# Optimization experiments

Hardware: AMD Instinct MI355X
Metric: run time of the kernel (lower is better)

## Reference

```python
import jax, jax.numpy as jnp
import numpy as np

N, E, G, H, D = 50000, 800000, 64, 2, 128  # nodes, edges, graphs, heads, out_channels
NEG_SLOPE_ATT = 0.2   # GATv2 default negative_slope
NEG_SLOPE_OUT = 0.01  # torch.nn.LeakyReLU default
BN_EPS = 1e-5


def setup_inputs() -> dict:
    key = jax.random.key(0)
    ks = jax.random.split(key, 12)
    x = jax.random.normal(ks[0], (N, 1), jnp.float32)
    edge_index = jax.random.randint(ks[1], (2, E), 0, N, dtype=jnp.int64)
    edge_attr = jax.random.normal(ks[2], (E,), jnp.float32)
    batch = jnp.sort(jax.random.randint(ks[3], (N,), 0, G, dtype=jnp.int64))
    # GATv2Conv params: lin_l/lin_r: Linear(1, H*D) with bias; lin_edge: Linear(1, H*D) no bias
    Wl = jax.random.normal(ks[4], (1, H * D), jnp.float32) * 0.5
    bl = jax.random.normal(ks[5], (H * D,), jnp.float32) * 0.1
    Wr = jax.random.normal(ks[6], (1, H * D), jnp.float32) * 0.5
    br = jax.random.normal(ks[7], (H * D,), jnp.float32) * 0.1
    We = jax.random.normal(ks[8], (1, H * D), jnp.float32) * 0.5
    att = jax.random.normal(ks[9], (H, D), jnp.float32) * 0.5
    bias = jax.random.normal(ks[10], (D,), jnp.float32) * 0.1
    gamma = jnp.ones((D,), jnp.float32)
    beta = jnp.zeros((D,), jnp.float32)
    return {"x": x, "edge_index": edge_index, "edge_attr": edge_attr, "batch": batch,
            "Wl": Wl, "bl": bl, "Wr": Wr, "br": br, "We": We, "att": att,
            "bias": bias, "gamma": gamma, "beta": beta}


def reference(x, edge_index, edge_attr, batch, Wl, bl, Wr, br, We, att, bias, gamma, beta):
    n = x.shape[0]
    src, dst = edge_index[0], edge_index[1]  # message flows src -> dst
    # node transforms: [N, H, D]
    xl = (x @ Wl + bl).reshape(n, H, D)  # lin_l (source side, also the message value)
    xr = (x @ Wr + br).reshape(n, H, D)  # lin_r (destination side)
    # edge feature embedding: [E, H, D]
    ee = (edge_attr[:, None] @ We).reshape(-1, H, D)
    # GATv2 scoring: leaky_relu(x_j + x_i + e), then dot with attention vector
    m = jax.nn.leaky_relu(xl[src] + xr[dst] + ee, NEG_SLOPE_ATT)  # [E, H, D]
    alpha = jnp.einsum('ehd,hd->eh', m, att)  # [E, H]
    # scatter-softmax over incoming edges per destination node
    amax = jax.ops.segment_max(alpha, dst, num_segments=n)  # [N, H]
    ea = jnp.exp(alpha - amax[dst])
    denom = jax.ops.segment_sum(ea, dst, num_segments=n)
    alpha = ea / (denom[dst] + 1e-16)
    # weighted scatter-add aggregation of x_j
    out = jax.ops.segment_sum(xl[src] * alpha[..., None], dst, num_segments=n)  # [N, H, D]
    out = out.mean(axis=1) + bias  # concat=False -> head average, then conv bias
    # BatchNorm1d in training mode (biased variance over nodes)
    mean = out.mean(axis=0)
    var = ((out - mean) ** 2).mean(axis=0)
    out = (out - mean) * jax.lax.rsqrt(var + BN_EPS) * gamma + beta
    out = jax.nn.leaky_relu(out, NEG_SLOPE_OUT)
    # graph-level scatter_add pooling
    return jax.ops.segment_sum(out, batch, num_segments=G)  # [G, D]
```

## Files before the change

### kernel.cpp

```cpp
#include <hip/hip_runtime.h>
#include <math.h>

#define NN 50000
#define NE 800000
#define NG 64

#define CB    1024
#define NBLK  782
#define NBUCK 196

static_assert(NBLK * CB >= NE, "chunk cover");
static_assert((NBUCK - 1) == (NN - 1) / 256, "bucket count");

#define WS_C     0
#define WS_ACC   16
#define WS_BNSUM (WS_ACC + 4*NN)
#define WS_BNSQ  (WS_BNSUM + 128)
#define WS_MOM   WS_BNSUM
#define WS_EX    (WS_BNSQ + 128)
#define WS_TOT   (WS_EX + 272)
#define WS_CNT   (WS_TOT + 256)
#define WS_REC0  (WS_CNT + 256*NBLK)
#define WS_SORT  (WS_REC0 + 4*NE)
#define WS_END   (WS_SORT + 4*NE)
#define WS_NEED_BYTES ((size_t)WS_END * 4 + 256)

static_assert(((WS_REC0 * 4) % 16) == 0, "rec0 16B alignment");
static_assert(((WS_SORT * 4) % 16) == 0, "sort 16B alignment");
static_assert(NE % 4 == 0, "edge unroll");

#define STEP(wl_, wr_, we_, bb_, at_, xs_, xd_, ae_, acc_)                 \
  { float tt = fmaf(we_, ae_, bb_); tt = fmaf(wr_, xd_, tt);               \
    tt = fmaf(wl_, xs_, tt); acc_ = fmaf(fabsf(tt), at_, acc_); }

#define SMEM_WEIGHTS_DECL                                                  \
  __shared__ __align__(16) float sWl[256], sWr[256], sWe[256], sB[256], sAt[256];

#define SMEM_WEIGHTS_LOAD                                                  \
  { int t_ = threadIdx.x;                                                  \
    sWl[t_] = Wl[t_]; sWr[t_] = Wr[t_]; sWe[t_] = We[t_];                  \
    sB[t_] = bl[t_] + br[t_]; sAt[t_] = att[t_]; }                         \
  __syncthreads();

#define SCORES(xs_, xd_, ae_, accA, accB, out0, out1)                      \
  { float lin0 = fmaf(c0.x, xs_, fmaf(c0.y, xd_, fmaf(c0.z, ae_, c0.w))); \
    out0 = fmaf(0.4f, accA, 0.6f * lin0);                                  \
    float lin1 = fmaf(c1.x, xs_, fmaf(c1.y, xd_, fmaf(c1.z, ae_, c1.w))); \
    out1 = fmaf(0.4f, accB, 0.6f * lin1); }

#define STEP4(c, q0, q1, q2, q3)                                           \
  STEP(wl.c, wr.c, we.c, bb.c, at.c, xs0, xd0, ae0, q0)                    \
  STEP(wl.c, wr.c, we.c, bb.c, at.c, xs1, xd1, ae1, q1)                    \
  STEP(wl.c, wr.c, we.c, bb.c, at.c, xs2, xd2, ae2, q2)                    \
  STEP(wl.c, wr.c, we.c, bb.c, at.c, xs3, xd3, ae3, q3)

#define SCORE_CORE                                                         \
  int4 s4 = *(const int4*)&ei[base];                                       \
  int4 dd4 = *(const int4*)&ei[NE + base];                                 \
  float4 ae4 = *(const float4*)&eattr[base];                               \
  float xs0 = x[s4.x], xs1 = x[s4.y], xs2 = x[s4.z], xs3 = x[s4.w];        \
  float xd0 = x[dd4.x], xd1 = x[dd4.y], xd2 = x[dd4.z], xd3 = x[dd4.w];    \
  float ae0 = ae4.x, ae1 = ae4.y, ae2 = ae4.z, ae3 = ae4.w;

#define SCORE_LOOPS                                                        \
  float a00 = 0.f, a01 = 0.f, a02 = 0.f, a03 = 0.f;                        \
  float a10 = 0.f, a11 = 0.f, a12 = 0.f, a13 = 0.f;                        \
  _Pragma("unroll 2")                                                      \
  for (int j = 0; j < 128; j += 4) {                                       \
    float4 wl = *(const float4*)&sWl[j];                                   \
    float4 wr = *(const float4*)&sWr[j];                                   \
    float4 we = *(const float4*)&sWe[j];                                   \
    float4 bb = *(const float4*)&sB[j];                                    \
    float4 at = *(const float4*)&sAt[j];                                   \
    STEP4(x, a00, a01, a02, a03)                                           \
    STEP4(y, a00, a01, a02, a03)                                           \
    STEP4(z, a00, a01, a02, a03)                                           \
    STEP4(w, a00, a01, a02, a03)                                           \
  }                                                                        \
  _Pragma("unroll 2")                                                      \
  for (int j = 128; j < 256; j += 4) {                                     \
    float4 wl = *(const float4*)&sWl[j];                                   \
    float4 wr = *(const float4*)&sWr[j];                                   \
    float4 we = *(const float4*)&sWe[j];                                   \
    float4 bb = *(const float4*)&sB[j];                                    \
    float4 at = *(const float4*)&sAt[j];                                   \
    STEP4(x, a10, a11, a12, a13)                                           \
    STEP4(y, a10, a11, a12, a13)                                           \
    STEP4(z, a10, a11, a12, a13)                                           \
    STEP4(w, a10, a11, a12, a13)                                           \
  }                                                                        \
  float4 c0 = *(const float4*)&ws[WS_C];                                   \
  float4 c1 = *(const float4*)&ws[WS_C + 4];

extern "C" __global__ __launch_bounds__(256)
void k0_init(float* __restrict__ ws,
             const float* __restrict__ att, const float* __restrict__ Wl,
             const float* __restrict__ Wr, const float* __restrict__ We,
             const float* __restrict__ bl, const float* __restrict__ br,
             float* __restrict__ out, int dense)
{
  int tid = blockIdx.x * 256 + threadIdx.x;
  int nt = gridDim.x * 256;
  if (dense) {
    if (tid < 14) ws[WS_MOM + tid] = 0.f;
  } else {
    for (int i = tid; i < 4 * NN; i += nt) ws[WS_ACC + i] = 0.f;
    for (int i = tid; i < 256; i += nt) ws[WS_BNSUM + i] = 0.f;
  }
  for (int i = tid; i < NG * 128; i += nt) out[i] = 0.f;
  if (blockIdx.x == 0) {
    __shared__ float red[4][256];
    int t = threadIdx.x;
    float a = att[t];
    red[0][t] = a * Wl[t];
    red[1][t] = a * Wr[t];
    red[2][t] = a * We[t];
    red[3][t] = a * (bl[t] + br[t]);
    __syncthreads();
    if (t < 8) {
      int k = t >> 1, h = t & 1;
      float s = 0.f;
      for (int d = 0; d < 128; ++d) s += red[k][h * 128 + d];
      ws[WS_C + h * 4 + k] = s;
    }
  }
}

extern "C" __global__ __launch_bounds__(256, 2)
void k_score(const int* __restrict__ ei, const float* __restrict__ x,
             const float* __restrict__ eattr,
             const float* __restrict__ Wl, const float* __restrict__ Wr,
             const float* __restrict__ We, const float* __restrict__ bl,
             const float* __restrict__ br, const float* __restrict__ att,
             float* __restrict__ ws)
{
  SMEM_WEIGHTS_DECL
  __shared__ unsigned cnt[256];
  cnt[threadIdx.x] = 0u;
  SMEM_WEIGHTS_LOAD
  int base = (blockIdx.x * 256 + threadIdx.x) * 4;
  if (base < NE) {
    SCORE_CORE
    atomicAdd(&cnt[((unsigned)dd4.x) >> 8], 1u);
    atomicAdd(&cnt[((unsigned)dd4.y) >> 8], 1u);
    atomicAdd(&cnt[((unsigned)dd4.z) >> 8], 1u);
    atomicAdd(&cnt[((unsigned)dd4.w) >> 8], 1u);
    SCORE_LOOPS
    float4* rec0 = (float4*)(ws + WS_REC0);
    float s0, s1;
    SCORES(xs0, xd0, ae0, a00, a10, s0, s1)
    rec0[base + 0] = make_float4(__expf(s0), __expf(s1), xs0, __uint_as_float((unsigned)dd4.x));
    SCORES(xs1, xd1, ae1, a01, a11, s0, s1)
    rec0[base + 1] = make_float4(__expf(s0), __expf(s1), xs1, __uint_as_float((unsigned)dd4.y));
    SCORES(xs2, xd2, ae2, a02, a12, s0, s1)
    rec0[base + 2] = make_float4(__expf(s0), __expf(s1), xs2, __uint_as_float((unsigned)dd4.z));
    SCORES(xs3, xd3, ae3, a03, a13, s0, s1)
    rec0[base + 3] = make_float4(__expf(s0), __expf(s1), xs3, __uint_as_float((unsigned)dd4.w));
  }
  __syncthreads();
  unsigned* counts = (unsigned*)(ws + WS_CNT);
  counts[(size_t)threadIdx.x * NBLK + blockIdx.x] = cnt[threadIdx.x];
}

extern "C" __global__ __launch_bounds__(256)
void k_scan1(float* __restrict__ ws)
{
  int b = blockIdx.x;
  int t = threadIdx.x;
  unsigned* row = (unsigned*)(ws + WS_CNT) + (size_t)b * NBLK;
  __shared__ unsigned sc[256];
  unsigned carry = 0;
  for (int c = 0; c < NBLK; c += 256) {
    int k = c + t;
    unsigned v = (k < NBLK) ? row[k] : 0u;
    sc[t] = v;
    __syncthreads();
    for (int o = 1; o < 256; o <<= 1) {
      unsigned u = (t >= o) ? sc[t - o] : 0u;
      __syncthreads();
      sc[t] += u;
      __syncthreads();
    }
    unsigned incl = sc[t];
    if (k < NBLK) row[k] = carry + incl - v;
    unsigned total = sc[255];
    __syncthreads();
    carry += total;
  }
  if (t == 0) ((unsigned*)(ws + WS_TOT))[b] = carry;
}

extern "C" __global__ __launch_bounds__(256)
void k_scan2(float* __restrict__ ws)
{
  int b = threadIdx.x;
  unsigned v = ((const unsigned*)(ws + WS_TOT))[b];
  __shared__ unsigned sc[256];
  sc[b] = v;
  __syncthreads();
  for (int o = 1; o < 256; o <<= 1) {
    unsigned u = (b >= o) ? sc[b - o] : 0u;
    __syncthreads();
    sc[b] += u;
    __syncthreads();
  }
  unsigned* ex = (unsigned*)(ws + WS_EX);
  ex[b] = sc[b] - v;
  if (b == 255) ex[256] = sc[b];
}

extern "C" __global__ __launch_bounds__(256)
void k_scatter(float* __restrict__ ws)
{
  __shared__ unsigned soff[256];
  int blk = blockIdx.x, tid = threadIdx.x;
  const unsigned* counts = (const unsigned*)(ws + WS_CNT);
  const unsigned* ex = (const unsigned*)(ws + WS_EX);
  soff[tid] = ex[tid] + counts[(size_t)tid * NBLK + blk];
  __syncthreads();
  const float4* rec0 = (const float4*)(ws + WS_REC0);
  float4* srt = (float4*)(ws + WS_SORT);
  int e0i = blk * CB + tid;
#pragma unroll
  for (int i = 0; i < 4; ++i) {
    int e = e0i + i * 256;
    if (e < NE) {
      float4 r = rec0[e];
      unsigned d = __float_as_uint(r.w);
      unsigned p = atomicAdd(&soff[d >> 8], 1u);
      srt[p] = r;
    }
  }
}

extern "C" __global__ __launch_bounds__(256)
void k_gather(float* __restrict__ ws)
{
  int b = blockIdx.x;
  const int t = threadIdx.x;
  __shared__ float acc[1024];
  acc[t] = 0.f; acc[256 + t] = 0.f; acc[512 + t] = 0.f; acc[768 + t] = 0.f;
  __syncthreads();
  const unsigned* ex = (const unsigned*)(ws + WS_EX);
  int lo = (int)ex[b], hi = (int)ex[b + 1];
  const float4* srt = (const float4*)(ws + WS_SORT);
  for (int i = lo + t; i < hi; i += 256) {
    float4 r = srt[i];
    int l4 = (int)(__float_as_uint(r.w) & 255u) * 4;
    atomicAdd(&acc[l4 + 0], r.x);
    atomicAdd(&acc[l4 + 1], r.y);
    atomicAdd(&acc[l4 + 2], r.x * r.z);
    atomicAdd(&acc[l4 + 3], r.y * r.z);
  }
  __syncthreads();
  int n = (b << 8) + t;
  float f1 = 0.f, f2 = 0.f, f3 = 0.f, f4 = 0.f;
  if (n < NN) {
    float4 A = make_float4(acc[t * 4], acc[t * 4 + 1], acc[t * 4 + 2], acc[t * 4 + 3]);
    *(float4*)&ws[WS_ACC + 4 * n] = A;
    float r0 = 1.f / (A.x + 1e-16f);
    float r1 = 1.f / (A.y + 1e-16f);
    f1 = A.x * r0; f2 = A.z * r0; f3 = A.y * r1; f4 = A.w * r1;
  }
  float pm[14] = { f1, f2, f3, f4,
                   f1*f1, f1*f2, f1*f3, f1*f4,
                   f2*f2, f2*f3, f2*f4,
                   f3*f3, f3*f4, f4*f4 };
#pragma unroll
  for (int k = 0; k < 14; ++k) {
    float v = pm[k];
#pragma unroll
    for (int m = 32; m >= 1; m >>= 1) v += __shfl_xor(v, m);
    pm[k] = v;
  }
  __shared__ float smom[56];
  int wid = t >> 6, lane = t & 63;
  if (lane == 0) {
#pragma unroll
    for (int k = 0; k < 14; ++k) smom[wid * 14 + k] = pm[k];
  }
  __syncthreads();
  if (t < 14) {
    float s = smom[t] + smom[14 + t] + smom[28 + t] + smom[42 + t];
    atomicAdd(&ws[WS_MOM + t], s);
  }
}

extern "C" __global__ __launch_bounds__(256)
void k4m_pool(const int* __restrict__ batch,
              const float* __restrict__ Wl, const float* __restrict__ bl,
              const float* __restrict__ bias, const float* __restrict__ gamma,
              const float* __restrict__ beta,
              float* __restrict__ ws, float* __restrict__ out)
{
  const int CHUNK = (NN + (int)gridDim.x - 1) / (int)gridDim.x;
  int n0 = blockIdx.x * CHUNK;
  if (n0 >= NN) return;
  int n1 = n0 + CHUNK; if (n1 > NN) n1 = NN;
  int t = threadIdx.x;
  int d = t & 127;
  int row = t >> 7;
  float S1 = ws[WS_MOM + 0], S2 = ws[WS_MOM + 1];
  float S3 = ws[WS_MOM + 2], S4 = ws[WS_MOM + 3];
  float M11 = ws[WS_MOM + 4], M12 = ws[WS_MOM + 5], M13 = ws[WS_MOM + 6];
  float M14 = ws[WS_MOM + 7], M22 = ws[WS_MOM + 8], M23 = ws[WS_MOM + 9];
  float M24 = ws[WS_MOM + 10], M33 = ws[WS_MOM + 11], M34 = ws[WS_MOM + 12];
  float M44 = ws[WS_MOM + 13];
  float g1 = 0.5f * bl[d], g2 = 0.5f * Wl[d];
  float g3 = 0.5f * bl[128 + d], g4 = 0.5f * Wl[128 + d];
  float g5 = bias[d];
  const float invN = 1.f / (float)NN;
  float dotS = g1 * S1 + g2 * S2 + g3 * S3 + g4 * S4;
  float mean = (dotS + (float)NN * g5) * invN;
  float sumsq = g1*g1*M11 + g2*g2*M22 + g3*g3*M33 + g4*g4*M44
              + 2.f*(g1*g2*M12 + g1*g3*M13 + g1*g4*M14
                   + g2*g3*M23 + g2*g4*M24 + g3*g4*M34)
              + 2.f*g5*dotS + (float)NN*g5*g5;
  float var = fmaf(sumsq, invN, -mean * mean);
  float scale = gamma[d] * rsqrtf(var + 1e-5f);
  float shift = fmaf(-mean, scale, beta[d]);
  __shared__ float pool[4][128];
  for (int i = t; i < 512; i += 256) ((float*)pool)[i] = 0.f;
  __syncthreads();
  int g0 = batch[n0];
  for (int n = n0 + row; n < n1; n += 2) {
    float4 a = *(const float4*)&ws[WS_ACC + 4 * n];
    float r0 = 1.f / (a.x + 1e-16f);
    float r1 = 1.f / (a.y + 1e-16f);
    float o = g1 * (a.x * r0) + g2 * (a.z * r0)
            + g3 * (a.y * r1) + g4 * (a.w * r1) + g5;
    float v = fmaf(o, scale, shift);
    v = v > 0.f ? v : 0.01f * v;
    int g = batch[n];
    int slot = g - g0;
    if (slot < 4) atomicAdd(&pool[slot][d], v);
    else atomicAdd(&out[g * 128 + d], v);
  }
  __syncthreads();
  for (int i = t; i < 512; i += 256) {
    int slot = i >> 7, dd = i & 127;
    int g = g0 + slot;
    float v = pool[slot][dd];
    if (g < NG && v != 0.f) atomicAdd(&out[g * 128 + dd], v);
  }
}

extern "C" __global__ __launch_bounds__(256)
void k12f(const int* __restrict__ ei, const float* __restrict__ x,
          const float* __restrict__ eattr,
          const float* __restrict__ Wl, const float* __restrict__ Wr,
          const float* __restrict__ We, const float* __restrict__ bl,
          const float* __restrict__ br, const float* __restrict__ att,
          float* __restrict__ ws)
{
  SMEM_WEIGHTS_DECL
  SMEM_WEIGHTS_LOAD
  int base = (blockIdx.x * 256 + threadIdx.x) * 4;
  if (base >= NE) return;
  SCORE_CORE
  SCORE_LOOPS
  float* acc = ws + WS_ACC;
  float s0, s1;
#define EPI2(xs_, xd_, ae_, accA, accB, dsti)                              \
  { SCORES(xs_, xd_, ae_, accA, accB, s0, s1)                              \
    float e0 = __expf(s0), e1 = __expf(s1);                                \
    float* a = &acc[4 * dsti];                                             \
    atomicAdd(a + 0, e0); atomicAdd(a + 1, e1);                            \
    atomicAdd(a + 2, e0 * xs_); atomicAdd(a + 3, e1 * xs_); }
  EPI2(xs0, xd0, ae0, a00, a10, dd4.x)
  EPI2(xs1, xd1, ae1, a01, a11, dd4.y)
  EPI2(xs2, xd2, ae2, a02, a12, dd4.z)
  EPI2(xs3, xd3, ae3, a03, a13, dd4.w)
#undef EPI2
}

__device__ __forceinline__ float node_out4(float4 a, float wl0, float wl1,
                                           float b0, float b1, float bs)
{
  float r0 = 1.f / (a.x + 1e-16f);
  float r1 = 1.f / (a.y + 1e-16f);
  return 0.5f * (fmaf(wl0, a.z * r0, b0 * (a.x * r0)) +
                 fmaf(wl1, a.w * r1, b1 * (a.y * r1))) + bs;
}

extern "C" __global__ __launch_bounds__(256)
void k3_stats(const float* __restrict__ Wl, const float* __restrict__ bl,
              const float* __restrict__ bias, float* __restrict__ ws)
{
  int d = threadIdx.x & 127;
  int row = threadIdx.x >> 7;
  float wl0 = Wl[d], wl1 = Wl[128 + d];
  float b0 = bl[d], b1 = bl[128 + d];
  float bs = bias[d];
  float sum = 0.f, sq = 0.f;
  for (int n = blockIdx.x * 2 + row; n < NN; n += gridDim.x * 2) {
    float4 a = *(const float4*)&ws[WS_ACC + 4 * n];
    float o = node_out4(a, wl0, wl1, b0, b1, bs);
    sum += o;
    sq = fmaf(o, o, sq);
  }
  __shared__ float l1[256], l2[256];
  l1[threadIdx.x] = sum; l2[threadIdx.x] = sq;
  __syncthreads();
  if (row == 0) {
    atomicAdd(&ws[WS_BNSUM + d], l1[d] + l1[128 + d]);
    atomicAdd(&ws[WS_BNSQ + d], l2[d] + l2[128 + d]);
  }
}

extern "C" __global__ __launch_bounds__(256)
void k4_pool(const int* __restrict__ batch,
             const float* __restrict__ Wl, const float* __restrict__ bl,
             const float* __restrict__ bias, const float* __restrict__ gamma,
             const float* __restrict__ beta,
             float* __restrict__ ws, float* __restrict__ out)
{
  const int CHUNK = (NN + (int)gridDim.x - 1) / (int)gridDim.x;
  int n0 = blockIdx.x * CHUNK;
  if (n0 >= NN) return;
  int n1 = n0 + CHUNK; if (n1 > NN) n1 = NN;
  int d = threadIdx.x & 127;
  int row = threadIdx.x >> 7;
  const float invN = 1.f / (float)NN;
  float mean = ws[WS_BNSUM + d] * invN;
  float var = fmaf(ws[WS_BNSQ + d], invN, -mean * mean);
  float scale = gamma[d] * rsqrtf(var + 1e-5f);
  float shift = fmaf(-mean, scale, beta[d]);
  float wl0 = Wl[d], wl1 = Wl[128 + d];
  float b0 = bl[d], b1 = bl[128 + d];
  float bs = bias[d];
  __shared__ float pool[4][128];
  for (int i = threadIdx.x; i < 512; i += 256) ((float*)pool)[i] = 0.f;
  __syncthreads();
  int g0 = batch[n0];
  for (int n = n0 + row; n < n1; n += 2) {
    float4 a = *(const float4*)&ws[WS_ACC + 4 * n];
    float o = node_out4(a, wl0, wl1, b0, b1, bs);
    float v = fmaf(o, scale, shift);
    v = v > 0.f ? v : 0.01f * v;
    int g = batch[n];
    int slot = g - g0;
    if (slot < 4) atomicAdd(&pool[slot][d], v);
    else atomicAdd(&out[g * 128 + d], v);
  }
  __syncthreads();
  for (int i = threadIdx.x; i < 512; i += 256) {
    int slot = i >> 7, dd = i & 127;
    int g = g0 + slot;
    float v = pool[slot][dd];
    if (g < NG && v != 0.f) atomicAdd(&out[g * 128 + dd], v);
  }
}

extern "C" void kernel_launch(void* const* d_in, const int* in_sizes, int n_in,
                              void* d_out, int out_size, void* d_ws, size_t ws_size,
                              hipStream_t stream) {
  const float* x     = (const float*)d_in[0];
  const int*   ei    = (const int*)d_in[1];
  const float* eattr = (const float*)d_in[2];
  const int*   batch = (const int*)d_in[3];
  const float* Wl    = (const float*)d_in[4];
  const float* bl    = (const float*)d_in[5];
  const float* Wr    = (const float*)d_in[6];
  const float* br    = (const float*)d_in[7];
  const float* We    = (const float*)d_in[8];
  const float* att   = (const float*)d_in[9];
  const float* bias  = (const float*)d_in[10];
  const float* gam   = (const float*)d_in[11];
  const float* bet   = (const float*)d_in[12];
  float* ws  = (float*)d_ws;
  float* out = (float*)d_out;

  const bool dense = (ws_size >= WS_NEED_BYTES);

  hipLaunchKernelGGL(k0_init, dim3(32), dim3(256), 0, stream,
                     ws, att, Wl, Wr, We, bl, br, out, dense ? 1 : 0);
  if (dense) {
    hipLaunchKernelGGL(k_score, dim3(NBLK), dim3(256), 0, stream,
                       ei, x, eattr, Wl, Wr, We, bl, br, att, ws);
    hipLaunchKernelGGL(k_scan1, dim3(256), dim3(256), 0, stream, ws);
    hipLaunchKernelGGL(k_scan2, dim3(1), dim3(256), 0, stream, ws);
    hipLaunchKernelGGL(k_scatter, dim3(NBLK), dim3(256), 0, stream, ws);
    hipLaunchKernelGGL(k_gather, dim3(NBUCK), dim3(256), 0, stream, ws);
    hipLaunchKernelGGL(k4m_pool, dim3(256), dim3(256), 0, stream,
                       batch, Wl, bl, bias, gam, bet, ws, out);
  } else {
    hipLaunchKernelGGL(k12f, dim3((NE / 4 + 255) / 256), dim3(256), 0, stream,
                       ei, x, eattr, Wl, Wr, We, bl, br, att, ws);
    hipLaunchKernelGGL(k3_stats, dim3(256), dim3(256), 0, stream,
                       Wl, bl, bias, ws);
    hipLaunchKernelGGL(k4_pool, dim3(256), dim3(256), 0, stream,
                       batch, Wl, bl, bias, gam, bet, ws, out);
  }
}
```

Measured before the change: 200.1 us.

## Histogram destinations first, then fuse scoring with bucket scatter

A lightweight histogram kernel now counts destination buckets per block and absorbs the init work, and the scans run before scoring. The score kernel then computes each edge's attention exponentials and writes the record straight into its sorted bucket slot. This removes the intermediate 12.8MB record buffer and the separate scatter pass. Each thread now handles 8 edges per block of 2048, which raises register pressure and halves the grid.

```diff
diff --git a/kernel.cpp b/kernel.cpp
--- a/kernel.cpp
+++ b/kernel.cpp
@@ -5,12 +5,13 @@
 #define NE 800000
 #define NG 64
 
-#define CB    1024
-#define NBLK  782
+#define CB    2048
+#define NBLK  391
 #define NBUCK 196
 
 static_assert(NBLK * CB >= NE, "chunk cover");
 static_assert((NBUCK - 1) == (NN - 1) / 256, "bucket count");
+static_assert(NE % 8 == 0, "edge unroll");
 
 #define WS_C     0
 #define WS_ACC   16
@@ -20,14 +21,11 @@
 #define WS_EX    (WS_BNSQ + 128)
 #define WS_TOT   (WS_EX + 272)
 #define WS_CNT   (WS_TOT + 256)
-#define WS_REC0  (WS_CNT + 256*NBLK)
-#define WS_SORT  (WS_REC0 + 4*NE)
+#define WS_SORT  (WS_CNT + 256*NBLK)
 #define WS_END   (WS_SORT + 4*NE)
 #define WS_NEED_BYTES ((size_t)WS_END * 4 + 256)
 
-static_assert(((WS_REC0 * 4) % 16) == 0, "rec0 16B alignment");
 static_assert(((WS_SORT * 4) % 16) == 0, "sort 16B alignment");
-static_assert(NE % 4 == 0, "edge unroll");
 
 #define STEP(wl_, wr_, we_, bb_, at_, xs_, xd_, ae_, acc_)                 \
   { float tt = fmaf(we_, ae_, bb_); tt = fmaf(wr_, xd_, tt);               \
@@ -92,22 +90,45 @@
   float4 c0 = *(const float4*)&ws[WS_C];                                   \
   float4 c1 = *(const float4*)&ws[WS_C + 4];
 
-extern "C" __global__ __launch_bounds__(256)
-void k0_init(float* __restrict__ ws,
-             const float* __restrict__ att, const float* __restrict__ Wl,
-             const float* __restrict__ Wr, const float* __restrict__ We,
-             const float* __restrict__ bl, const float* __restrict__ br,
-             float* __restrict__ out, int dense)
-{
-  int tid = blockIdx.x * 256 + threadIdx.x;
-  int nt = gridDim.x * 256;
-  if (dense) {
-    if (tid < 14) ws[WS_MOM + tid] = 0.f;
-  } else {
-    for (int i = tid; i < 4 * NN; i += nt) ws[WS_ACC + i] = 0.f;
-    for (int i = tid; i < 256; i += nt) ws[WS_BNSUM + i] = 0.f;
-  }
-  for (int i = tid; i < NG * 128; i += nt) out[i] = 0.f;
+#define STEP8(c, Q)                                                        \
+  STEP(wl.c, wr.c, we.c, bb.c, at.c, xs0, xd0, ae0, Q##0)                  \
+  STEP(wl.c, wr.c, we.c, bb.c, at.c, xs1, xd1, ae1, Q##1)                  \
+  STEP(wl.c, wr.c, we.c, bb.c, at.c, xs2, xd2, ae2, Q##2)                  \
+  STEP(wl.c, wr.c, we.c, bb.c, at.c, xs3, xd3, ae3, Q##3)                  \
+  STEP(wl.c, wr.c, we.c, bb.c, at.c, xs4, xd4, ae4, Q##4)                  \
+  STEP(wl.c, wr.c, we.c, bb.c, at.c, xs5, xd5, ae5, Q##5)                  \
+  STEP(wl.c, wr.c, we.c, bb.c, at.c, xs6, xd6, ae6, Q##6)                  \
+  STEP(wl.c, wr.c, we.c, bb.c, at.c, xs7, xd7, ae7, Q##7)
+
+extern "C" __global__ __launch_bounds__(256)
+void k_hist(const int* __restrict__ ei,
+            const float* __restrict__ att, const float* __restrict__ Wl,
+            const float* __restrict__ Wr, const float* __restrict__ We,
+            const float* __restrict__ bl, const float* __restrict__ br,
+            float* __restrict__ ws, float* __restrict__ out)
+{
+  __shared__ unsigned cnt[256];
+  cnt[threadIdx.x] = 0u;
+  __syncthreads();
+  int base = blockIdx.x * CB + (int)threadIdx.x * 8;
+  if (base < NE) {
+    int4 a = *(const int4*)&ei[NE + base];
+    int4 b = *(const int4*)&ei[NE + base + 4];
+    atomicAdd(&cnt[((unsigned)a.x) >> 8], 1u);
+    atomicAdd(&cnt[((unsigned)a.y) >> 8], 1u);
+    atomicAdd(&cnt[((unsigned)a.z) >> 8], 1u);
+    atomicAdd(&cnt[((unsigned)a.w) >> 8], 1u);
+    atomicAdd(&cnt[((unsigned)b.x) >> 8], 1u);
+    atomicAdd(&cnt[((unsigned)b.y) >> 8], 1u);
+    atomicAdd(&cnt[((unsigned)b.z) >> 8], 1u);
+    atomicAdd(&cnt[((unsigned)b.w) >> 8], 1u);
+  }
+  __syncthreads();
+  unsigned* counts = (unsigned*)(ws + WS_CNT);
+  counts[(size_t)threadIdx.x * NBLK + blockIdx.x] = cnt[threadIdx.x];
+  int gid = blockIdx.x * 256 + (int)threadIdx.x;
+  if (gid < NG * 128) out[gid] = 0.f;
+  if (gid < 14) ws[WS_MOM + gid] = 0.f;
   if (blockIdx.x == 0) {
     __shared__ float red[4][256];
     int t = threadIdx.x;
@@ -124,42 +145,6 @@
       ws[WS_C + h * 4 + k] = s;
     }
   }
-}
-
-extern "C" __global__ __launch_bounds__(256, 2)
-void k_score(const int* __restrict__ ei, const float* __restrict__ x,
-             const float* __restrict__ eattr,
-             const float* __restrict__ Wl, const float* __restrict__ Wr,
-             const float* __restrict__ We, const float* __restrict__ bl,
-             const float* __restrict__ br, const float* __restrict__ att,
-             float* __restrict__ ws)
-{
-  SMEM_WEIGHTS_DECL
-  __shared__ unsigned cnt[256];
-  cnt[threadIdx.x] = 0u;
-  SMEM_WEIGHTS_LOAD
-  int base = (blockIdx.x * 256 + threadIdx.x) * 4;
-  if (base < NE) {
-    SCORE_CORE
-    atomicAdd(&cnt[((unsigned)dd4.x) >> 8], 1u);
-    atomicAdd(&cnt[((unsigned)dd4.y) >> 8], 1u);
-    atomicAdd(&cnt[((unsigned)dd4.z) >> 8], 1u);
-    atomicAdd(&cnt[((unsigned)dd4.w) >> 8], 1u);
-    SCORE_LOOPS
-    float4* rec0 = (float4*)(ws + WS_REC0);
-    float s0, s1;
-    SCORES(xs0, xd0, ae0, a00, a10, s0, s1)
-    rec0[base + 0] = make_float4(__expf(s0), __expf(s1), xs0, __uint_as_float((unsigned)dd4.x));
-    SCORES(xs1, xd1, ae1, a01, a11, s0, s1)
-    rec0[base + 1] = make_float4(__expf(s0), __expf(s1), xs1, __uint_as_float((unsigned)dd4.y));
-    SCORES(xs2, xd2, ae2, a02, a12, s0, s1)
-    rec0[base + 2] = make_float4(__expf(s0), __expf(s1), xs2, __uint_as_float((unsigned)dd4.z));
-    SCORES(xs3, xd3, ae3, a03, a13, s0, s1)
-    rec0[base + 3] = make_float4(__expf(s0), __expf(s1), xs3, __uint_as_float((unsigned)dd4.w));
-  }
-  __syncthreads();
-  unsigned* counts = (unsigned*)(ws + WS_CNT);
-  counts[(size_t)threadIdx.x * NBLK + blockIdx.x] = cnt[threadIdx.x];
 }
 
 extern "C" __global__ __launch_bounds__(256)
@@ -209,28 +194,72 @@
   if (b == 255) ex[256] = sc[b];
 }
 
-extern "C" __global__ __launch_bounds__(256)
-void k_scatter(float* __restrict__ ws)
-{
+extern "C" __global__ __launch_bounds__(256, 2)
+void k_score(const int* __restrict__ ei, const float* __restrict__ x,
+             const float* __restrict__ eattr,
+             const float* __restrict__ Wl, const float* __restrict__ Wr,
+             const float* __restrict__ We, const float* __restrict__ bl,
+             const float* __restrict__ br, const float* __restrict__ att,
+             float* __restrict__ ws)
+{
+  SMEM_WEIGHTS_DECL
   __shared__ unsigned soff[256];
-  int blk = blockIdx.x, tid = threadIdx.x;
-  const unsigned* counts = (const unsigned*)(ws + WS_CNT);
-  const unsigned* ex = (const unsigned*)(ws + WS_EX);
-  soff[tid] = ex[tid] + counts[(size_t)tid * NBLK + blk];
-  __syncthreads();
-  const float4* rec0 = (const float4*)(ws + WS_REC0);
+  { int t_ = threadIdx.x;
+    sWl[t_] = Wl[t_]; sWr[t_] = Wr[t_]; sWe[t_] = We[t_];
+    sB[t_] = bl[t_] + br[t_]; sAt[t_] = att[t_];
+    const unsigned* counts = (const unsigned*)(ws + WS_CNT);
+    const unsigned* ex = (const unsigned*)(ws + WS_EX);
+    soff[t_] = ex[t_] + counts[(size_t)t_ * NBLK + blockIdx.x];
+  }
+  __syncthreads();
+  int base = blockIdx.x * CB + (int)threadIdx.x * 8;
+  if (base >= NE) return;
+  int4 sa = *(const int4*)&ei[base];
+  int4 sb = *(const int4*)&ei[base + 4];
+  int4 da = *(const int4*)&ei[NE + base];
+  int4 db = *(const int4*)&ei[NE + base + 4];
+  float4 aea = *(const float4*)&eattr[base];
+  float4 aeb = *(const float4*)&eattr[base + 4];
+  float ae0 = aea.x, ae1 = aea.y, ae2 = aea.z, ae3 = aea.w;
+  float ae4 = aeb.x, ae5 = aeb.y, ae6 = aeb.z, ae7 = aeb.w;
+  float xs0 = x[sa.x], xs1 = x[sa.y], xs2 = x[sa.z], xs3 = x[sa.w];
+  float xs4 = x[sb.x], xs5 = x[sb.y], xs6 = x[sb.z], xs7 = x[sb.w];
+  float xd0 = x[da.x], xd1 = x[da.y], xd2 = x[da.z], xd3 = x[da.w];
+  float xd4 = x[db.x], xd5 = x[db.y], xd6 = x[db.z], xd7 = x[db.w];
+  float q0 = 0.f, q1 = 0.f, q2 = 0.f, q3 = 0.f;
+  float q4 = 0.f, q5 = 0.f, q6 = 0.f, q7 = 0.f;
+  float r0 = 0.f, r1 = 0.f, r2 = 0.f, r3 = 0.f;
+  float r4 = 0.f, r5 = 0.f, r6 = 0.f, r7 = 0.f;
+#pragma unroll 2
+  for (int j = 0; j < 128; j += 4) {
+    float4 wl = *(const float4*)&sWl[j];
+    float4 wr = *(const float4*)&sWr[j];
+    float4 we = *(const float4*)&sWe[j];
+    float4 bb = *(const float4*)&sB[j];
+    float4 at = *(const float4*)&sAt[j];
+    STEP8(x, q) STEP8(y, q) STEP8(z, q) STEP8(w, q)
+  }
+#pragma unroll 2
+  for (int j = 128; j < 256; j += 4) {
+    float4 wl = *(const float4*)&sWl[j];
+    float4 wr = *(const float4*)&sWr[j];
+    float4 we = *(const float4*)&sWe[j];
+    float4 bb = *(const float4*)&sB[j];
+    float4 at = *(const float4*)&sAt[j];
+    STEP8(x, r) STEP8(y, r) STEP8(z, r) STEP8(w, r)
+  }
+  float4 c0 = *(const float4*)&ws[WS_C];
+  float4 c1 = *(const float4*)&ws[WS_C + 4];
   float4* srt = (float4*)(ws + WS_SORT);
-  int e0i = blk * CB + tid;
-#pragma unroll
-  for (int i = 0; i < 4; ++i) {
-    int e = e0i + i * 256;
-    if (e < NE) {
-      float4 r = rec0[e];
-      unsigned d = __float_as_uint(r.w);
-      unsigned p = atomicAdd(&soff[d >> 8], 1u);
-      srt[p] = r;
-    }
-  }
+  float s0, s1;
+#define EPI(i, dv)                                                         \
+  { SCORES(xs##i, xd##i, ae##i, q##i, r##i, s0, s1)                        \
+    unsigned d_ = (unsigned)(dv);                                          \
+    unsigned p_ = atomicAdd(&soff[d_ >> 8], 1u);                           \
+    srt[p_] = make_float4(__expf(s0), __expf(s1), xs##i, __uint_as_float(d_)); }
+  EPI(0, da.x) EPI(1, da.y) EPI(2, da.z) EPI(3, da.w)
+  EPI(4, db.x) EPI(5, db.y) EPI(6, db.z) EPI(7, db.w)
+#undef EPI
 }
 
 extern "C" __global__ __launch_bounds__(256)
@@ -346,6 +375,36 @@
 }
 
 extern "C" __global__ __launch_bounds__(256)
+void k0_init(float* __restrict__ ws,
+             const float* __restrict__ att, const float* __restrict__ Wl,
+             const float* __restrict__ Wr, const float* __restrict__ We,
+             const float* __restrict__ bl, const float* __restrict__ br,
+             float* __restrict__ out)
+{
+  int tid = blockIdx.x * 256 + threadIdx.x;
+  int nt = gridDim.x * 256;
+  for (int i = tid; i < 4 * NN; i += nt) ws[WS_ACC + i] = 0.f;
+  for (int i = tid; i < 256; i += nt) ws[WS_BNSUM + i] = 0.f;
+  for (int i = tid; i < NG * 128; i += nt) out[i] = 0.f;
+  if (blockIdx.x == 0) {
+    __shared__ float red[4][256];
+    int t = threadIdx.x;
+    float a = att[t];
+    red[0][t] = a * Wl[t];
+    red[1][t] = a * Wr[t];
+    red[2][t] = a * We[t];
+    red[3][t] = a * (bl[t] + br[t]);
+    __syncthreads();
+    if (t < 8) {
+      int k = t >> 1, h = t & 1;
+      float s = 0.f;
+      for (int d = 0; d < 128; ++d) s += red[k][h * 128 + d];
+      ws[WS_C + h * 4 + k] = s;
+    }
+  }
+}
+
+extern "C" __global__ __launch_bounds__(256)
 void k12f(const int* __restrict__ ei, const float* __restrict__ x,
           const float* __restrict__ eattr,
           const float* __restrict__ Wl, const float* __restrict__ Wr,
@@ -473,18 +532,19 @@
 
   const bool dense = (ws_size >= WS_NEED_BYTES);
 
-  hipLaunchKernelGGL(k0_init, dim3(32), dim3(256), 0, stream,
-                     ws, att, Wl, Wr, We, bl, br, out, dense ? 1 : 0);
   if (dense) {
+    hipLaunchKernelGGL(k_hist, dim3(NBLK), dim3(256), 0, stream,
+                       ei, att, Wl, Wr, We, bl, br, ws, out);
+    hipLaunchKernelGGL(k_scan1, dim3(256), dim3(256), 0, stream, ws);
+    hipLaunchKernelGGL(k_scan2, dim3(1), dim3(256), 0, stream, ws);
     hipLaunchKernelGGL(k_score, dim3(NBLK), dim3(256), 0, stream,
                        ei, x, eattr, Wl, Wr, We, bl, br, att, ws);
-    hipLaunchKernelGGL(k_scan1, dim3(256), dim3(256), 0, stream, ws);
-    hipLaunchKernelGGL(k_scan2, dim3(1), dim3(256), 0, stream, ws);
-    hipLaunchKernelGGL(k_scatter, dim3(NBLK), dim3(256), 0, stream, ws);
     hipLaunchKernelGGL(k_gather, dim3(NBUCK), dim3(256), 0, stream, ws);
     hipLaunchKernelGGL(k4m_pool, dim3(256), dim3(256), 0, stream,
                        batch, Wl, bl, bias, gam, bet, ws, out);
   } else {
+    hipLaunchKernelGGL(k0_init, dim3(128), dim3(256), 0, stream,
+                       ws, att, Wl, Wr, We, bl, br, out);
     hipLaunchKernelGGL(k12f, dim3((NE / 4 + 255) / 256), dim3(256), 0, stream,
                        ei, x, eattr, Wl, Wr, We, bl, br, att, ws);
     hipLaunchKernelGGL(k3_stats, dim3(256), dim3(256), 0, stream,
```

New measurement: 188.4 us. 1.06x faster.
